# Kernel optimization log

Hardware: AMD Instinct MI355X
Metric: run time of the kernel (lower is better)

Reference implementation:

```python
import jax, jax.numpy as jnp
import numpy as np

HEADS = 32
DK = 32            # att_size = hidden // heads
CUT = 15.5         # tot_dis[cur_layer=0] + 0.5
NEG = -1e8
LN_EPS = 1e-5


def layernorm(x, g, b):
    m = jnp.mean(x, axis=-1, keepdims=True)
    v = jnp.mean((x - m) ** 2, axis=-1, keepdims=True)
    return (x - m) / jnp.sqrt(v + LN_EPS) * g + b


def setup_inputs() -> dict:
    key = jax.random.key(0)
    ks = jax.random.split(key, 12)
    B, S, H, F = 8, 513, 1024, 4096
    N = S - 1
    def nrm(k, shape, scale=0.02):
        return jax.random.normal(k, shape, jnp.float32) * scale
    x = jax.random.normal(ks[0], (B, S, H), jnp.float32)
    attn_bias = jax.random.normal(ks[1], (B, HEADS, S, S), jnp.float32)
    rel_pos = jax.random.randint(ks[2], (B, N, N), 0, 16, jnp.int32)
    rel_emb = nrm(ks[3], (512, HEADS)).at[0].set(0.0)  # padding_idx=0
    Wq = nrm(ks[4], (H, H)); bq = jnp.zeros((H,), jnp.float32)
    Wk = nrm(ks[5], (H, H)); bk = jnp.zeros((H,), jnp.float32)
    Wv = nrm(ks[6], (H, H)); bv = jnp.zeros((H,), jnp.float32)
    Wo = nrm(ks[7], (H, H)); bo = jnp.zeros((H,), jnp.float32)
    W1 = nrm(ks[8], (H, F)); b1 = jnp.zeros((F,), jnp.float32)
    W2 = nrm(ks[9], (F, H)); b2 = jnp.zeros((H,), jnp.float32)
    ln1_g = jnp.ones((H,), jnp.float32); ln1_b = jnp.zeros((H,), jnp.float32)
    ln2_g = jnp.ones((H,), jnp.float32); ln2_b = jnp.zeros((H,), jnp.float32)
    return dict(x=x, attn_bias=attn_bias, rel_emb=rel_emb,
                Wq=Wq, bq=bq, Wk=Wk, bk=bk, Wv=Wv, bv=bv, Wo=Wo, bo=bo,
                W1=W1, b1=b1, W2=W2, b2=b2,
                ln1_g=ln1_g, ln1_b=ln1_b, ln2_g=ln2_g, ln2_b=ln2_b,
                rel_pos=rel_pos)


def reference(x, attn_bias, rel_emb, Wq, bq, Wk, bk, Wv, bv, Wo, bo,
              W1, b1, W2, b2, ln1_g, ln1_b, ln2_g, ln2_b, rel_pos):
    B, S, H = x.shape
    # rel-pos bias: embed [B,N,N] -> [B,N,N,heads] -> [B,heads,N,N]
    rpb = jnp.transpose(rel_emb[rel_pos], (0, 3, 1, 2))
    inner = attn_bias[:, :, 1:, 1:] + rpb
    # per-head mask flag: keep if within cutoff distance OR already -inf-masked
    flags = (rel_pos[:, None, :, :] <= CUT) | (inner < NEG)
    ab = attn_bias.at[:, :, 1:, 1:].set(inner * flags)
    # attention
    y = layernorm(x, ln1_g, ln1_b)
    scale = DK ** -0.5
    q = (y @ Wq + bq).reshape(B, S, HEADS, DK) * scale
    k = (y @ Wk + bk).reshape(B, S, HEADS, DK)
    v = (y @ Wv + bv).reshape(B, S, HEADS, DK)
    scores = jnp.einsum('bqhd,bkhd->bhqk', q, k) + ab
    attn = jax.nn.softmax(scores, axis=-1)
    o = jnp.einsum('bhqk,bkhd->bqhd', attn, v).reshape(B, S, H)
    x = x + (o @ Wo + bo)
    # FFN
    y = layernorm(x, ln2_g, ln2_b)
    y = jax.nn.gelu(y @ W1 + b1, approximate=False) @ W2 + b2
    return x + y
```

## Files before the change

kernel.cpp:

```cpp
#include <hip/hip_runtime.h>
#include <hip/hip_bf16.h>
#include <math.h>

typedef __attribute__((ext_vector_type(8))) short short8;
typedef __attribute__((ext_vector_type(4))) float f32x4;
typedef unsigned short u16;
typedef unsigned int u32;

#define SQ 513
#define MPAD 4224
#define MV 4104
#define NHEADS 32
#define DKH 32
#define SVP 576

static __device__ inline u16 f2bf(float f) {
  u32 u = __builtin_bit_cast(u32, f);
  u = (u + 0x7fffu + ((u >> 16) & 1u)) >> 16;
  return (u16)u;
}

static __device__ inline void gld16(const void* g, void* l) {
  __builtin_amdgcn_global_load_lds((__attribute__((address_space(1))) void*)g,
                                   (__attribute__((address_space(3))) void*)l,
                                   16, 0, 0);
}

static __device__ inline float gelu_f(float x) {
  return 0.5f * x * (1.f + erff(x * 0.70710678118654752f));
}

__global__ __launch_bounds__(256) void transpose_cast_k(const float* __restrict__ in,
    u16* __restrict__ out, int K, int N, float scale)
{
  __shared__ float t[32][33];
  int n0 = blockIdx.x * 32, k0 = blockIdx.y * 32;
  int tx = threadIdx.x & 31, ty = threadIdx.x >> 5;
#pragma unroll
  for (int i = 0; i < 32; i += 8)
    t[ty + i][tx] = in[(size_t)(k0 + ty + i) * N + n0 + tx];
  __syncthreads();
#pragma unroll
  for (int i = 0; i < 32; i += 8)
    out[(size_t)(n0 + ty + i) * K + k0 + tx] = f2bf(t[tx][ty + i] * scale);
}

__global__ __launch_bounds__(256) void vtrans_k(const u16* __restrict__ qkv,
    u16* __restrict__ vT)
{
  __shared__ u16 t[32][33];
  int st = blockIdx.x * 32, h = blockIdx.y, b = blockIdx.z;
  int tx = threadIdx.x & 31, ty = threadIdx.x >> 5;
#pragma unroll
  for (int i = 0; i < 32; i += 8) {
    int s = st + ty + i;
    int sc = s > 512 ? 512 : s;
    t[ty + i][tx] = qkv[(size_t)(b * SQ + sc) * 3072 + 2048 + h * DKH + tx];
  }
  __syncthreads();
#pragma unroll
  for (int i = 0; i < 32; i += 8) {
    int d = ty + i;
    vT[(((size_t)b * NHEADS + h) * DKH + d) * SVP + st + tx] = t[tx][d];
  }
}

__global__ __launch_bounds__(256) void prep_bias_k(const float* __restrict__ bq,
    const float* __restrict__ bk, const float* __restrict__ bv,
    float* __restrict__ out, float scale)
{
  int i = blockIdx.x * 256 + threadIdx.x;
  float v = (i < 1024) ? bq[i] * scale : ((i < 2048) ? bk[i - 1024] : bv[i - 2048]);
  out[i] = v;
}

__global__ __launch_bounds__(256) void ln_k(const float* __restrict__ in,
    const float* __restrict__ g, const float* __restrict__ b,
    u16* __restrict__ out)
{
  int row = blockIdx.x;
  float4 v = ((const float4*)(in + (size_t)row * 1024))[threadIdx.x];
  float s = v.x + v.y + v.z + v.w;
  float s2 = v.x * v.x + v.y * v.y + v.z * v.z + v.w * v.w;
#pragma unroll
  for (int d = 32; d; d >>= 1) { s += __shfl_xor(s, d, 64); s2 += __shfl_xor(s2, d, 64); }
  __shared__ float ps[4], ps2[4];
  int w = threadIdx.x >> 6;
  if ((threadIdx.x & 63) == 0) { ps[w] = s; ps2[w] = s2; }
  __syncthreads();
  s = ps[0] + ps[1] + ps[2] + ps[3];
  s2 = ps2[0] + ps2[1] + ps2[2] + ps2[3];
  float mean = s * (1.f / 1024.f);
  float var = s2 * (1.f / 1024.f) - mean * mean;
  float inv = rsqrtf(var + 1e-5f);
  float4 gv = ((const float4*)g)[threadIdx.x];
  float4 bv = ((const float4*)b)[threadIdx.x];
  ushort4 o;
  o.x = f2bf((v.x - mean) * inv * gv.x + bv.x);
  o.y = f2bf((v.y - mean) * inv * gv.y + bv.y);
  o.z = f2bf((v.z - mean) * inv * gv.z + bv.z);
  o.w = f2bf((v.w - mean) * inv * gv.w + bv.w);
  ((ushort4*)(out + (size_t)row * 1024))[threadIdx.x] = o;
}

template <int EPI>
__global__ __launch_bounds__(256) void gemm_bt(const u16* __restrict__ A,
    const u16* __restrict__ Bw, const float* __restrict__ bias,
    const float* __restrict__ resid, void* __restrict__ outp,
    int N, int K, int nbx)
{
  __shared__ alignas(16) u16 sA[128 * 64];
  __shared__ alignas(16) u16 sB[128 * 64];
  int tid = threadIdx.x;
  int l = tid & 63, lg = l >> 4, li = l & 15;

  int bidx = blockIdx.x;
  int kbeg = 0, kend = K;
  float* pout = (float*)outp;
  if (EPI == 4) {
    int half = gridDim.x >> 1;
    int s = bidx >= half;
    bidx -= s * half;
    kbeg = s * (K >> 1);
    kend = kbeg + (K >> 1);
    pout += (size_t)s * MPAD * 1024;
  }
  int mb = bidx / nbx, nb = bidx % nbx;
  int m0 = mb * 128, n0 = nb * 128;
  int wv = tid >> 6;
  int wr = wv >> 1, wc = wv & 1;
  f32x4 acc[4][4] = {};
  int r_ = tid >> 3, c_ = (tid & 7) * 8;
  const u16* Ag = A + (size_t)(m0 + r_) * K + c_;
  const u16* Bg = Bw + (size_t)(n0 + r_) * K + c_;
  u16* sAb = sA + (tid & 192) * 8;
  u16* sBb = sB + (tid & 192) * 8;

  for (int k0 = kbeg; k0 < kend; k0 += 64) {
    __syncthreads();
#pragma unroll
    for (int i = 0; i < 4; ++i) {
      gld16(Ag + (size_t)(i * 32) * K + k0, sAb + i * 2048);
      gld16(Bg + (size_t)(i * 32) * K + k0, sBb + i * 2048);
    }
    __syncthreads();
#pragma unroll
    for (int ks = 0; ks < 2; ++ks) {
      short8 af[4], bfr[4];
#pragma unroll
      for (int i = 0; i < 4; ++i)
        af[i] = *(const short8*)&sA[(64 * wr + 16 * i + li) * 64 + ks * 32 + lg * 8];
#pragma unroll
      for (int j = 0; j < 4; ++j)
        bfr[j] = *(const short8*)&sB[(64 * wc + 16 * j + li) * 64 + ks * 32 + lg * 8];
#pragma unroll
      for (int i = 0; i < 4; ++i)
#pragma unroll
        for (int j = 0; j < 4; ++j)
          acc[i][j] = __builtin_amdgcn_mfma_f32_16x16x32_bf16(af[i], bfr[j], acc[i][j], 0, 0, 0);
    }
  }

#pragma unroll
  for (int i = 0; i < 4; ++i) {
    int rb = m0 + 64 * wr + 16 * i + 4 * lg;
#pragma unroll
    for (int j = 0; j < 4; ++j) {
      int col = n0 + 64 * wc + 16 * j + li;
      float bia = (EPI == 4) ? 0.f : bias[col];
#pragma unroll
      for (int r = 0; r < 4; ++r) {
        int row = rb + r;
        float v = acc[i][j][r] + bia;
        if (EPI == 0) {
          ((u16*)outp)[(size_t)row * N + col] = f2bf(v);
        } else if (EPI == 2) {
          ((u16*)outp)[(size_t)row * N + col] = f2bf(gelu_f(v));
        } else {
          pout[(size_t)row * N + col] = v;
        }
      }
    }
  }
}

__global__ __launch_bounds__(256) void oproj_combine(const float* __restrict__ part,
    float* __restrict__ out, const float* __restrict__ bo, const float* __restrict__ x)
{
  size_t idx = (size_t)blockIdx.x * 256 + threadIdx.x;
  const float4* p0 = (const float4*)part;
  const float4* p1 = (const float4*)(part + (size_t)MPAD * 1024);
  float4 a = p0[idx], b = p1[idx];
  float4 bb = ((const float4*)bo)[idx & 255];
  float4 xx = ((const float4*)x)[idx];
  a.x += b.x + bb.x + xx.x;
  a.y += b.y + bb.y + xx.y;
  a.z += b.z + bb.z + xx.z;
  a.w += b.w + bb.w + xx.w;
  ((float4*)out)[idx] = a;
}

__global__ __launch_bounds__(256) void ffn2_combine(const float* __restrict__ part,
    float* __restrict__ out, const float* __restrict__ b2)
{
  size_t idx = (size_t)blockIdx.x * 256 + threadIdx.x;
  const float4* p0 = (const float4*)part;
  const float4* p1 = (const float4*)(part + (size_t)MPAD * 1024);
  float4 a = ((float4*)out)[idx];
  float4 x0 = p0[idx], x1 = p1[idx];
  float4 bb = ((const float4*)b2)[idx & 255];
  a.x += x0.x + x1.x + bb.x;
  a.y += x0.y + x1.y + bb.y;
  a.z += x0.z + x1.z + bb.z;
  a.w += x0.w + x1.w + bb.w;
  ((float4*)out)[idx] = a;
}

__global__ __launch_bounds__(256) void attn_fused(const u16* __restrict__ qkv,
    const u16* __restrict__ vT, const float* __restrict__ attn_bias,
    const int* __restrict__ rel_pos, const float* __restrict__ rel_emb,
    u16* __restrict__ o)
{
  __shared__ alignas(16) u16 k_lds[2][64 * 32];
  __shared__ alignas(16) u16 v_lds[2][32 * 64];
  __shared__ alignas(16) u16 p_lds[4][16][72];
  int bid = blockIdx.x;
  int qt = bid % 9, h = (bid / 9) % NHEADS, b = bid / (9 * NHEADS);
  int tid = threadIdx.x, wv = tid >> 6, l = tid & 63, lg = l >> 4, li = l & 15;
  int q0 = qt * 64;
  int sqb = q0 + 16 * wv + 4 * lg;

  short8 qfrag = *(const short8*)(qkv + (size_t)(b * SQ + q0 + 16 * wv + li) * 3072 + h * DKH + lg * 8);

  float tv = rel_emb[(size_t)li * NHEADS + h];

  const float* bias_row[4];
  const int* rp_row[4];
#pragma unroll
  for (int r = 0; r < 4; ++r) {
    int sq = sqb + r;
    int sqc = sq > 512 ? 512 : sq;
    bias_row[r] = attn_bias + (((size_t)b * NHEADS + h) * SQ + sqc) * SQ;
    int sqm = sq - 1; sqm = sqm < 0 ? 0 : (sqm > 511 ? 511 : sqm);
    rp_row[r] = rel_pos + ((size_t)b * 512 + sqm) * 512;
  }

  int krow = tid >> 2;
  int kchunk = (tid & 3) ^ ((tid >> 3) & 3);
  const u16* ksrc = qkv + (size_t)(b * SQ) * 3072 + 1024 + h * DKH + kchunk * 8;
  int vrow = tid >> 3;
  int vchunk = (tid & 7) ^ (vrow & 7);
  const u16* vsrc = vT + (((size_t)b * NHEADS + h) * DKH + vrow) * SVP + vchunk * 8;

  int koff[4], voff[4];
#pragma unroll
  for (int f = 0; f < 4; ++f)
    koff[f] = (16 * f + li) * 32 + ((lg ^ ((li >> 1) & 3)) * 8);
#pragma unroll
  for (int u = 0; u < 4; ++u) {
    int df = u >> 1, kk = u & 1;
    voff[u] = (16 * df + li) * 64 + (((kk * 4 + lg) ^ (li & 7)) * 8);
  }

  float pb[4][4];
  int pr[4][4];

  gld16(ksrc + (size_t)krow * 3072, (u16*)k_lds[0] + tid * 8);
  gld16(vsrc, (u16*)v_lds[0] + tid * 8);
  __builtin_amdgcn_sched_barrier(0);
#pragma unroll
  for (int f = 0; f < 4; ++f) {
    int sk = 16 * f + li;
    int skm = sk - 1; skm = skm < 0 ? 0 : skm;
#pragma unroll
    for (int r = 0; r < 4; ++r) {
      pb[f][r] = bias_row[r][sk];
      pr[f][r] = rp_row[r][skm];
    }
  }

  f32x4 o_acc[2] = {};
  float l_run[4] = {0.f, 0.f, 0.f, 0.f};

#pragma unroll 1
  for (int kt = 0; kt < 9; ++kt) {
    int cur = kt & 1;
    asm volatile("s_waitcnt vmcnt(32)" ::: "memory");
    __builtin_amdgcn_s_barrier();
    if (kt < 8) {
      int s = (kt + 1) * 64 + krow; if (s > 512) s = 512;
      gld16(ksrc + (size_t)s * 3072, (u16*)k_lds[cur ^ 1] + tid * 8);
      gld16(vsrc + (size_t)(kt + 1) * 64, (u16*)v_lds[cur ^ 1] + tid * 8);
    }
    __builtin_amdgcn_sched_barrier(0);
    const u16* kb = k_lds[cur];
    const u16* vbf = v_lds[cur];

    f32x4 sc[4];
    __builtin_amdgcn_s_setprio(1);
#pragma unroll
    for (int f = 0; f < 4; ++f) {
      short8 kf = *(const short8*)&kb[koff[f]];
      f32x4 z = {};
      sc[f] = __builtin_amdgcn_mfma_f32_16x16x32_bf16(qfrag, kf, z, 0, 0, 0);
    }
    __builtin_amdgcn_s_setprio(0);

#pragma unroll
    for (int f = 0; f < 4; ++f) {
      int sk = kt * 64 + 16 * f + li;
#pragma unroll
      for (int r = 0; r < 4; ++r) {
        int sq = sqb + r;
        float base = pb[f][r];
        int rp = pr[f][r];
        float re = __shfl(tv, rp, 64);
        float inner = base + re;
        float ab = (rp <= 15 || inner < -1e8f) ? inner : 0.f;
        if (sq == 0 || sk == 0) ab = base;
        if (sq > 512 || sk > 512) ab = -1e30f;
        sc[f][r] += ab;
      }
    }
    if (kt < 8) {
#pragma unroll
      for (int f = 0; f < 4; ++f) {
        int sk = (kt + 1) * 64 + 16 * f + li;
        int skc = sk > 512 ? 512 : sk;
        int skm = sk - 1; skm = skm > 511 ? 511 : skm;
#pragma unroll
        for (int r = 0; r < 4; ++r) {
          pb[f][r] = bias_row[r][skc];
          pr[f][r] = rp_row[r][skm];
        }
      }
    }

#pragma unroll
    for (int f = 0; f < 4; ++f)
#pragma unroll
      for (int r = 0; r < 4; ++r) {
        float p = __expf(sc[f][r]);
        l_run[r] += p;
        p_lds[wv][4 * lg + r][16 * f + li] = f2bf(p);
      }

    __builtin_amdgcn_s_setprio(1);
#pragma unroll
    for (int kk = 0; kk < 2; ++kk) {
      short8 pa = *(const short8*)&p_lds[wv][li][kk * 32 + lg * 8];
#pragma unroll
      for (int df = 0; df < 2; ++df) {
        short8 vb = *(const short8*)&vbf[voff[df * 2 + kk]];
        o_acc[df] = __builtin_amdgcn_mfma_f32_16x16x32_bf16(pa, vb, o_acc[df], 0, 0, 0);
      }
    }
    __builtin_amdgcn_s_setprio(0);
  }

#pragma unroll
  for (int r = 0; r < 4; ++r) {
    float s = l_run[r];
#pragma unroll
    for (int d = 1; d < 16; d <<= 1) s += __shfl_xor(s, d, 16);
    l_run[r] = s;
  }
#pragma unroll
  for (int df = 0; df < 2; ++df)
#pragma unroll
    for (int r = 0; r < 4; ++r) {
      int s_q = sqb + r;
      if (s_q <= 512)
        o[(size_t)(b * SQ + s_q) * 1024 + h * DKH + 16 * df + li] = f2bf(o_acc[df][r] / l_run[r]);
    }
}

extern "C" void kernel_launch(void* const* d_in, const int* in_sizes, int n_in,
                              void* d_out, int out_size, void* d_ws, size_t ws_size,
                              hipStream_t stream) {
  const float* x        = (const float*)d_in[0];
  const float* attn_bias= (const float*)d_in[1];
  const float* rel_emb  = (const float*)d_in[2];
  const float* Wq = (const float*)d_in[3];
  const float* bq = (const float*)d_in[4];
  const float* Wk = (const float*)d_in[5];
  const float* bk = (const float*)d_in[6];
  const float* Wv = (const float*)d_in[7];
  const float* bv = (const float*)d_in[8];
  const float* Wo = (const float*)d_in[9];
  const float* bo = (const float*)d_in[10];
  const float* W1 = (const float*)d_in[11];
  const float* b1 = (const float*)d_in[12];
  const float* W2 = (const float*)d_in[13];
  const float* b2 = (const float*)d_in[14];
  const float* ln1g = (const float*)d_in[15];
  const float* ln1b = (const float*)d_in[16];
  const float* ln2g = (const float*)d_in[17];
  const float* ln2b = (const float*)d_in[18];
  const int*   rel_pos = (const int*)d_in[19];
  float* out = (float*)d_out;

  char* ws = (char*)d_ws;
  size_t off = 0;
  auto alloc = [&](size_t bytes) { char* p = ws + off; off += (bytes + 255) & ~(size_t)255; return p; };
  u16* w_qkvT = (u16*)alloc((size_t)3072 * 1024 * 2);
  u16* w_oT   = (u16*)alloc((size_t)1024 * 1024 * 2);
  u16* w_1T   = (u16*)alloc((size_t)4096 * 1024 * 2);
  u16* w_2T   = (u16*)alloc((size_t)1024 * 4096 * 2);
  float* bias_qkv = (float*)alloc(3072 * 4);
  u16* ybuf = (u16*)alloc((size_t)MPAD * 1024 * 2);
  u16* obuf = (u16*)alloc((size_t)MPAD * 1024 * 2);
  u16* vTb  = (u16*)alloc((size_t)8 * NHEADS * DKH * SVP * 2);
  u16* big  = (u16*)alloc((size_t)MPAD * 4096 * 2);
  float* part = (float*)alloc((size_t)2 * MPAD * 1024 * 4);

  const float scale = 0.17677669529663689f;
  dim3 blk(256);

  transpose_cast_k<<<dim3(32, 32), blk, 0, stream>>>(Wq, w_qkvT, 1024, 1024, scale);
  transpose_cast_k<<<dim3(32, 32), blk, 0, stream>>>(Wk, w_qkvT + (size_t)1024 * 1024, 1024, 1024, 1.f);
  transpose_cast_k<<<dim3(32, 32), blk, 0, stream>>>(Wv, w_qkvT + (size_t)2048 * 1024, 1024, 1024, 1.f);
  transpose_cast_k<<<dim3(32, 32), blk, 0, stream>>>(Wo, w_oT, 1024, 1024, 1.f);
  transpose_cast_k<<<dim3(128, 32), blk, 0, stream>>>(W1, w_1T, 1024, 4096, 1.f);
  transpose_cast_k<<<dim3(32, 128), blk, 0, stream>>>(W2, w_2T, 4096, 1024, 1.f);
  prep_bias_k<<<12, blk, 0, stream>>>(bq, bk, bv, bias_qkv, scale);

  ln_k<<<MV, blk, 0, stream>>>(x, ln1g, ln1b, ybuf);
  gemm_bt<0><<<33 * 24, blk, 0, stream>>>(ybuf, w_qkvT, bias_qkv, nullptr, big, 3072, 1024, 24);
  vtrans_k<<<dim3(18, NHEADS, 8), blk, 0, stream>>>(big, vTb);
  attn_fused<<<8 * NHEADS * 9, blk, 0, stream>>>(big, vTb, attn_bias, rel_pos, rel_emb, obuf);
  gemm_bt<4><<<33 * 8 * 2, blk, 0, stream>>>(obuf, w_oT, bo, nullptr, part, 1024, 1024, 8);
  oproj_combine<<<MV, blk, 0, stream>>>(part, out, bo, x);
  ln_k<<<MV, blk, 0, stream>>>(out, ln2g, ln2b, ybuf);
  gemm_bt<2><<<33 * 32, blk, 0, stream>>>(ybuf, w_1T, b1, nullptr, big, 4096, 1024, 32);
  gemm_bt<4><<<33 * 8 * 2, blk, 0, stream>>>(big, w_2T, b2, nullptr, part, 1024, 4096, 8);
  ffn2_combine<<<MV, blk, 0, stream>>>(part, out, b2);
}
```

Measured before the change: 492.0 us.

## Split attention key range across two blocks and combine partial results

Each attention block now handles only half of the key tiles (0-4 or 5-8), which doubles the grid to improve occupancy and parallelism. It writes unnormalized fp32 partial outputs and row sums to workspace, and a new combine kernel adds them, normalizes and casts to bf16. The softmax uses plain exp without a running max, so partials can be added directly. This adds an extra kernel launch and fp32 partial traffic, and the pipeline wait is now a full __syncthreads with no explicit vmcnt.

```diff
diff --git a/kernel.cpp b/kernel.cpp
--- a/kernel.cpp
+++ b/kernel.cpp
@@ -13,6 +13,7 @@
 #define NHEADS 32
 #define DKH 32
 #define SVP 576
+#define SQP 576
 
 static __device__ inline u16 f2bf(float f) {
   u32 u = __builtin_bit_cast(u32, f);
@@ -216,16 +217,39 @@
   ((float4*)out)[idx] = a;
 }
 
+__global__ __launch_bounds__(256) void attn_combine(const float* __restrict__ opart,
+    const float* __restrict__ lpart, u16* __restrict__ o)
+{
+  int row = blockIdx.x;
+  int b = row / SQ, sq = row % SQ;
+  int t = threadIdx.x;
+  int h = t >> 3;
+  float l0 = lpart[((size_t)b * NHEADS + h) * SQP + sq];
+  float l1 = lpart[(((size_t)8 + b) * NHEADS + h) * SQP + sq];
+  float inv = 1.f / (l0 + l1);
+  float4 o0 = ((const float4*)(opart + ((size_t)b * SQP + sq) * 1024))[t];
+  float4 o1 = ((const float4*)(opart + (((size_t)8 + b) * SQP + sq) * 1024))[t];
+  ushort4 r;
+  r.x = f2bf((o0.x + o1.x) * inv);
+  r.y = f2bf((o0.y + o1.y) * inv);
+  r.z = f2bf((o0.z + o1.z) * inv);
+  r.w = f2bf((o0.w + o1.w) * inv);
+  ((ushort4*)(o + (size_t)row * 1024))[t] = r;
+}
+
 __global__ __launch_bounds__(256) void attn_fused(const u16* __restrict__ qkv,
     const u16* __restrict__ vT, const float* __restrict__ attn_bias,
     const int* __restrict__ rel_pos, const float* __restrict__ rel_emb,
-    u16* __restrict__ o)
+    float* __restrict__ opart, float* __restrict__ lpart)
 {
   __shared__ alignas(16) u16 k_lds[2][64 * 32];
   __shared__ alignas(16) u16 v_lds[2][32 * 64];
   __shared__ alignas(16) u16 p_lds[4][16][72];
   int bid = blockIdx.x;
-  int qt = bid % 9, h = (bid / 9) % NHEADS, b = bid / (9 * NHEADS);
+  int sh = bid & 1;
+  int t3 = bid >> 1;
+  int qt = t3 % 9, h = (t3 / 9) % NHEADS, b = t3 / (9 * NHEADS);
+  int kb = sh ? 5 : 0, ke = sh ? 9 : 5;
   int tid = threadIdx.x, wv = tid >> 6, l = tid & 63, lg = l >> 4, li = l & 15;
   int q0 = qt * 64;
   int sqb = q0 + 16 * wv + 4 * lg;
@@ -265,12 +289,11 @@
   float pb[4][4];
   int pr[4][4];
 
-  gld16(ksrc + (size_t)krow * 3072, (u16*)k_lds[0] + tid * 8);
-  gld16(vsrc, (u16*)v_lds[0] + tid * 8);
-  __builtin_amdgcn_sched_barrier(0);
+  gld16(ksrc + (size_t)(kb * 64 + krow) * 3072, (u16*)k_lds[0] + tid * 8);
+  gld16(vsrc + (size_t)(kb * 64), (u16*)v_lds[0] + tid * 8);
 #pragma unroll
   for (int f = 0; f < 4; ++f) {
-    int sk = 16 * f + li;
+    int sk = kb * 64 + 16 * f + li;
     int skm = sk - 1; skm = skm < 0 ? 0 : skm;
 #pragma unroll
     for (int r = 0; r < 4; ++r) {
@@ -283,24 +306,22 @@
   float l_run[4] = {0.f, 0.f, 0.f, 0.f};
 
 #pragma unroll 1
-  for (int kt = 0; kt < 9; ++kt) {
-    int cur = kt & 1;
-    asm volatile("s_waitcnt vmcnt(32)" ::: "memory");
-    __builtin_amdgcn_s_barrier();
-    if (kt < 8) {
+  for (int kt = kb; kt < ke; ++kt) {
+    int cur = (kt - kb) & 1;
+    __syncthreads();
+    if (kt + 1 < ke) {
       int s = (kt + 1) * 64 + krow; if (s > 512) s = 512;
       gld16(ksrc + (size_t)s * 3072, (u16*)k_lds[cur ^ 1] + tid * 8);
       gld16(vsrc + (size_t)(kt + 1) * 64, (u16*)v_lds[cur ^ 1] + tid * 8);
     }
-    __builtin_amdgcn_sched_barrier(0);
-    const u16* kb = k_lds[cur];
+    const u16* kbp = k_lds[cur];
     const u16* vbf = v_lds[cur];
 
     f32x4 sc[4];
     __builtin_amdgcn_s_setprio(1);
 #pragma unroll
     for (int f = 0; f < 4; ++f) {
-      short8 kf = *(const short8*)&kb[koff[f]];
+      short8 kf = *(const short8*)&kbp[koff[f]];
       f32x4 z = {};
       sc[f] = __builtin_amdgcn_mfma_f32_16x16x32_bf16(qfrag, kf, z, 0, 0, 0);
     }
@@ -322,7 +343,7 @@
         sc[f][r] += ab;
       }
     }
-    if (kt < 8) {
+    if (kt + 1 < ke) {
 #pragma unroll
       for (int f = 0; f < 4; ++f) {
         int sk = (kt + 1) * 64 + 16 * f + li;
@@ -365,14 +386,18 @@
     for (int d = 1; d < 16; d <<= 1) s += __shfl_xor(s, d, 16);
     l_run[r] = s;
   }
-#pragma unroll
-  for (int df = 0; df < 2; ++df)
-#pragma unroll
-    for (int r = 0; r < 4; ++r) {
-      int s_q = sqb + r;
-      if (s_q <= 512)
-        o[(size_t)(b * SQ + s_q) * 1024 + h * DKH + 16 * df + li] = f2bf(o_acc[df][r] / l_run[r]);
-    }
+  float* ob = opart + ((size_t)(sh * 8 + b) * SQP) * 1024 + h * DKH;
+#pragma unroll
+  for (int r = 0; r < 4; ++r) {
+    int s_q = sqb + r;
+    if (s_q <= 512) {
+#pragma unroll
+      for (int df = 0; df < 2; ++df)
+        ob[(size_t)s_q * 1024 + 16 * df + li] = o_acc[df][r];
+      if (li == 0)
+        lpart[(((size_t)sh * 8 + b) * NHEADS + h) * SQP + s_q] = l_run[r];
+    }
+  }
 }
 
 extern "C" void kernel_launch(void* const* d_in, const int* in_sizes, int n_in,
@@ -412,7 +437,9 @@
   u16* obuf = (u16*)alloc((size_t)MPAD * 1024 * 2);
   u16* vTb  = (u16*)alloc((size_t)8 * NHEADS * DKH * SVP * 2);
   u16* big  = (u16*)alloc((size_t)MPAD * 4096 * 2);
-  float* part = (float*)alloc((size_t)2 * MPAD * 1024 * 4);
+  float* part  = (float*)alloc((size_t)2 * MPAD * 1024 * 4);
+  float* opart = (float*)alloc((size_t)16 * SQP * 1024 * 4);
+  float* lpart = (float*)alloc((size_t)16 * NHEADS * SQP * 4);
 
   const float scale = 0.17677669529663689f;
   dim3 blk(256);
@@ -428,7 +455,8 @@
   ln_k<<<MV, blk, 0, stream>>>(x, ln1g, ln1b, ybuf);
   gemm_bt<0><<<33 * 24, blk, 0, stream>>>(ybuf, w_qkvT, bias_qkv, nullptr, big, 3072, 1024, 24);
   vtrans_k<<<dim3(18, NHEADS, 8), blk, 0, stream>>>(big, vTb);
-  attn_fused<<<8 * NHEADS * 9, blk, 0, stream>>>(big, vTb, attn_bias, rel_pos, rel_emb, obuf);
+  attn_fused<<<8 * NHEADS * 9 * 2, blk, 0, stream>>>(big, vTb, attn_bias, rel_pos, rel_emb, opart, lpart);
+  attn_combine<<<8 * SQ, blk, 0, stream>>>(opart, lpart, obuf);
   gemm_bt<4><<<33 * 8 * 2, blk, 0, stream>>>(obuf, w_oT, bo, nullptr, part, 1024, 1024, 8);
   oproj_combine<<<MV, blk, 0, stream>>>(part, out, bo, x);
   ln_k<<<MV, blk, 0, stream>>>(out, ln2g, ln2b, ybuf);
```

Measured after the change: 507.7 us. +3.2%, slower.

## Precompute masked attention bias as tiled fp16 and stream it into LDS

Applied to the files above, without the earlier changes.

Adds a prep kernel that folds the attention bias, relative-position embedding lookup and cutoff mask into one fp16 tensor laid out per 64-key tile. The attention kernel then streams these tiles into double-buffered LDS with global_load_lds instead of doing scattered fp32 bias and rel_pos loads and shuffles per element. It also swaps the MFMA operand order so each lane holds four consecutive keys, which allows vectorized bias reads and P stores. This costs an extra pass over the full bias tensor and clamps the bias to the fp16 range, which can change results where masked values sit near the limit.

```diff
diff --git a/kernel.cpp b/kernel.cpp
--- a/kernel.cpp
+++ b/kernel.cpp
@@ -13,6 +13,7 @@
 #define NHEADS 32
 #define DKH 32
 #define SVP 576
+#define SQP 576
 
 static __device__ inline u16 f2bf(float f) {
   u32 u = __builtin_bit_cast(u32, f);
@@ -20,6 +21,14 @@
   return (u16)u;
 }
 
+static __device__ inline u16 f2h(float f) {
+  _Float16 h = (_Float16)f;
+  return __builtin_bit_cast(u16, h);
+}
+static __device__ inline float h2f(u16 b) {
+  return (float)__builtin_bit_cast(_Float16, b);
+}
+
 static __device__ inline void gld16(const void* g, void* l) {
   __builtin_amdgcn_global_load_lds((__attribute__((address_space(1))) void*)g,
                                    (__attribute__((address_space(3))) void*)l,
@@ -62,6 +71,39 @@
   for (int i = 0; i < 32; i += 8) {
     int d = ty + i;
     vT[(((size_t)b * NHEADS + h) * DKH + d) * SVP + st + tx] = t[tx][d];
+  }
+}
+
+__global__ __launch_bounds__(256) void prep_ab(const float* __restrict__ attn_bias,
+    const int* __restrict__ rel_pos, const float* __restrict__ rel_emb,
+    u16* __restrict__ abt)
+{
+  int bh = blockIdx.x;
+  int b = bh >> 5, h = bh & 31;
+  int t = threadIdx.x;
+  const float* brow_base = attn_bias + ((size_t)bh * SQ) * SQ;
+#pragma unroll 1
+  for (int rl = 0; rl < 16; ++rl) {
+    int sq = blockIdx.y * 16 + rl;
+#pragma unroll
+    for (int cc = 0; cc < 3; ++cc) {
+      int sk = t + cc * 256;
+      if (sk >= SQP) continue;
+      float ab;
+      if (sq > 512 || sk > 512) ab = -30000.f;
+      else {
+        float base = brow_base[(size_t)sq * SQ + sk];
+        if (sq == 0 || sk == 0) ab = base;
+        else {
+          int rp = rel_pos[((size_t)b * 512 + sq - 1) * 512 + sk - 1];
+          float inner = base + rel_emb[(size_t)rp * NHEADS + h];
+          ab = (rp <= 15 || inner < -1e8f) ? inner : 0.f;
+          if (ab < -30000.f) ab = -30000.f;
+        }
+      }
+      int kt = sk >> 6, kp = sk & 63;
+      abt[(((size_t)bh * 9 + kt) * SQP + sq) * 64 + kp] = f2h(ab);
+    }
   }
 }
 
@@ -217,13 +259,14 @@
 }
 
 __global__ __launch_bounds__(256) void attn_fused(const u16* __restrict__ qkv,
-    const u16* __restrict__ vT, const float* __restrict__ attn_bias,
-    const int* __restrict__ rel_pos, const float* __restrict__ rel_emb,
+    const u16* __restrict__ vT, const u16* __restrict__ abt,
     u16* __restrict__ o)
 {
   __shared__ alignas(16) u16 k_lds[2][64 * 32];
   __shared__ alignas(16) u16 v_lds[2][32 * 64];
+  __shared__ alignas(16) u16 ab_lds[2][64 * 64];
   __shared__ alignas(16) u16 p_lds[4][16][72];
+  __shared__ float l_lds[4][16];
   int bid = blockIdx.x;
   int qt = bid % 9, h = (bid / 9) % NHEADS, b = bid / (9 * NHEADS);
   int tid = threadIdx.x, wv = tid >> 6, l = tid & 63, lg = l >> 4, li = l & 15;
@@ -231,19 +274,6 @@
   int sqb = q0 + 16 * wv + 4 * lg;
 
   short8 qfrag = *(const short8*)(qkv + (size_t)(b * SQ + q0 + 16 * wv + li) * 3072 + h * DKH + lg * 8);
-
-  float tv = rel_emb[(size_t)li * NHEADS + h];
-
-  const float* bias_row[4];
-  const int* rp_row[4];
-#pragma unroll
-  for (int r = 0; r < 4; ++r) {
-    int sq = sqb + r;
-    int sqc = sq > 512 ? 512 : sq;
-    bias_row[r] = attn_bias + (((size_t)b * NHEADS + h) * SQ + sqc) * SQ;
-    int sqm = sq - 1; sqm = sqm < 0 ? 0 : (sqm > 511 ? 511 : sqm);
-    rp_row[r] = rel_pos + ((size_t)b * 512 + sqm) * 512;
-  }
 
   int krow = tid >> 2;
   int kchunk = (tid & 3) ^ ((tid >> 3) & 3);
@@ -251,99 +281,77 @@
   int vrow = tid >> 3;
   int vchunk = (tid & 7) ^ (vrow & 7);
   const u16* vsrc = vT + (((size_t)b * NHEADS + h) * DKH + vrow) * SVP + vchunk * 8;
-
-  int koff[4], voff[4];
+  int abrow = tid >> 3;
+  int abcir = (tid & 7) ^ (abrow & 7);
+  const u16* absrc0 = abt + ((size_t)(b * NHEADS + h) * 9) * SQP * 64 + (size_t)q0 * 64
+                      + abrow * 64 + abcir * 8;
+
+  int koff[4];
 #pragma unroll
   for (int f = 0; f < 4; ++f)
     koff[f] = (16 * f + li) * 32 + ((lg ^ ((li >> 1) & 3)) * 8);
+  int voff[4];
 #pragma unroll
   for (int u = 0; u < 4; ++u) {
     int df = u >> 1, kk = u & 1;
     voff[u] = (16 * df + li) * 64 + (((kk * 4 + lg) ^ (li & 7)) * 8);
   }
-
-  float pb[4][4];
-  int pr[4][4];
+  int aboff[4];
+#pragma unroll
+  for (int f = 0; f < 4; ++f)
+    aboff[f] = (16 * wv + li) * 128 + (((2 * f + (lg >> 1)) ^ (li & 7)) << 4) + 8 * (lg & 1);
 
   gld16(ksrc + (size_t)krow * 3072, (u16*)k_lds[0] + tid * 8);
   gld16(vsrc, (u16*)v_lds[0] + tid * 8);
-  __builtin_amdgcn_sched_barrier(0);
-#pragma unroll
-  for (int f = 0; f < 4; ++f) {
-    int sk = 16 * f + li;
-    int skm = sk - 1; skm = skm < 0 ? 0 : skm;
-#pragma unroll
-    for (int r = 0; r < 4; ++r) {
-      pb[f][r] = bias_row[r][sk];
-      pr[f][r] = rp_row[r][skm];
-    }
-  }
+  gld16(absrc0, (u16*)ab_lds[0] + tid * 8);
+  gld16(absrc0 + 2048, (u16*)ab_lds[0] + 2048 + tid * 8);
 
   f32x4 o_acc[2] = {};
-  float l_run[4] = {0.f, 0.f, 0.f, 0.f};
+  float l_run = 0.f;
 
 #pragma unroll 1
   for (int kt = 0; kt < 9; ++kt) {
     int cur = kt & 1;
-    asm volatile("s_waitcnt vmcnt(32)" ::: "memory");
-    __builtin_amdgcn_s_barrier();
+    __syncthreads();
     if (kt < 8) {
       int s = (kt + 1) * 64 + krow; if (s > 512) s = 512;
       gld16(ksrc + (size_t)s * 3072, (u16*)k_lds[cur ^ 1] + tid * 8);
       gld16(vsrc + (size_t)(kt + 1) * 64, (u16*)v_lds[cur ^ 1] + tid * 8);
-    }
-    __builtin_amdgcn_sched_barrier(0);
-    const u16* kb = k_lds[cur];
+      const u16* abn = absrc0 + (size_t)(kt + 1) * SQP * 64;
+      gld16(abn, (u16*)ab_lds[cur ^ 1] + tid * 8);
+      gld16(abn + 2048, (u16*)ab_lds[cur ^ 1] + 2048 + tid * 8);
+    }
+    const u16* kbp = k_lds[cur];
     const u16* vbf = v_lds[cur];
+    const char* abl = (const char*)ab_lds[cur];
 
     f32x4 sc[4];
     __builtin_amdgcn_s_setprio(1);
 #pragma unroll
     for (int f = 0; f < 4; ++f) {
-      short8 kf = *(const short8*)&kb[koff[f]];
+      short8 kf = *(const short8*)&kbp[koff[f]];
       f32x4 z = {};
-      sc[f] = __builtin_amdgcn_mfma_f32_16x16x32_bf16(qfrag, kf, z, 0, 0, 0);
+      sc[f] = __builtin_amdgcn_mfma_f32_16x16x32_bf16(kf, qfrag, z, 0, 0, 0);
     }
     __builtin_amdgcn_s_setprio(0);
 
 #pragma unroll
     for (int f = 0; f < 4; ++f) {
-      int sk = kt * 64 + 16 * f + li;
-#pragma unroll
-      for (int r = 0; r < 4; ++r) {
-        int sq = sqb + r;
-        float base = pb[f][r];
-        int rp = pr[f][r];
-        float re = __shfl(tv, rp, 64);
-        float inner = base + re;
-        float ab = (rp <= 15 || inner < -1e8f) ? inner : 0.f;
-        if (sq == 0 || sk == 0) ab = base;
-        if (sq > 512 || sk > 512) ab = -1e30f;
-        sc[f][r] += ab;
-      }
-    }
-    if (kt < 8) {
-#pragma unroll
-      for (int f = 0; f < 4; ++f) {
-        int sk = (kt + 1) * 64 + 16 * f + li;
-        int skc = sk > 512 ? 512 : sk;
-        int skm = sk - 1; skm = skm > 511 ? 511 : skm;
-#pragma unroll
-        for (int r = 0; r < 4; ++r) {
-          pb[f][r] = bias_row[r][skc];
-          pr[f][r] = rp_row[r][skm];
-        }
-      }
-    }
-
-#pragma unroll
-    for (int f = 0; f < 4; ++f)
-#pragma unroll
-      for (int r = 0; r < 4; ++r) {
-        float p = __expf(sc[f][r]);
-        l_run[r] += p;
-        p_lds[wv][4 * lg + r][16 * f + li] = f2bf(p);
-      }
+      uint2 uu = *(const uint2*)(abl + aboff[f]);
+      float a0 = h2f((u16)(uu.x & 0xffffu));
+      float a1 = h2f((u16)(uu.x >> 16));
+      float a2 = h2f((u16)(uu.y & 0xffffu));
+      float a3 = h2f((u16)(uu.y >> 16));
+      float p0 = __expf(sc[f][0] + a0);
+      float p1 = __expf(sc[f][1] + a1);
+      float p2 = __expf(sc[f][2] + a2);
+      float p3 = __expf(sc[f][3] + a3);
+      l_run += (p0 + p1) + (p2 + p3);
+      uint2 pk;
+      pk.x = (u32)f2bf(p0) | ((u32)f2bf(p1) << 16);
+      pk.y = (u32)f2bf(p2) | ((u32)f2bf(p3) << 16);
+      *(uint2*)((char*)&p_lds[wv][0][0] + li * 144 + f * 32 + lg * 8) = pk;
+    }
 
     __builtin_amdgcn_s_setprio(1);
 #pragma unroll
@@ -358,20 +366,20 @@
     __builtin_amdgcn_s_setprio(0);
   }
 
-#pragma unroll
-  for (int r = 0; r < 4; ++r) {
-    float s = l_run[r];
-#pragma unroll
-    for (int d = 1; d < 16; d <<= 1) s += __shfl_xor(s, d, 16);
-    l_run[r] = s;
-  }
+  float s = l_run;
+  s += __shfl_xor(s, 16, 64);
+  s += __shfl_xor(s, 32, 64);
+  if (l < 16) l_lds[wv][l] = s;
+  float lr[4];
+#pragma unroll
+  for (int r = 0; r < 4; ++r) lr[r] = l_lds[wv][4 * lg + r];
 #pragma unroll
   for (int df = 0; df < 2; ++df)
 #pragma unroll
     for (int r = 0; r < 4; ++r) {
       int s_q = sqb + r;
       if (s_q <= 512)
-        o[(size_t)(b * SQ + s_q) * 1024 + h * DKH + 16 * df + li] = f2bf(o_acc[df][r] / l_run[r]);
+        o[(size_t)(b * SQ + s_q) * 1024 + h * DKH + 16 * df + li] = f2bf(o_acc[df][r] / lr[r]);
     }
 }
 
@@ -413,10 +421,12 @@
   u16* vTb  = (u16*)alloc((size_t)8 * NHEADS * DKH * SVP * 2);
   u16* big  = (u16*)alloc((size_t)MPAD * 4096 * 2);
   float* part = (float*)alloc((size_t)2 * MPAD * 1024 * 4);
+  u16* abt  = (u16*)alloc((size_t)256 * 9 * SQP * 64 * 2);
 
   const float scale = 0.17677669529663689f;
   dim3 blk(256);
 
+  prep_ab<<<dim3(256, 36), blk, 0, stream>>>(attn_bias, rel_pos, rel_emb, abt);
   transpose_cast_k<<<dim3(32, 32), blk, 0, stream>>>(Wq, w_qkvT, 1024, 1024, scale);
   transpose_cast_k<<<dim3(32, 32), blk, 0, stream>>>(Wk, w_qkvT + (size_t)1024 * 1024, 1024, 1024, 1.f);
   transpose_cast_k<<<dim3(32, 32), blk, 0, stream>>>(Wv, w_qkvT + (size_t)2048 * 1024, 1024, 1024, 1.f);
@@ -428,7 +438,7 @@
   ln_k<<<MV, blk, 0, stream>>>(x, ln1g, ln1b, ybuf);
   gemm_bt<0><<<33 * 24, blk, 0, stream>>>(ybuf, w_qkvT, bias_qkv, nullptr, big, 3072, 1024, 24);
   vtrans_k<<<dim3(18, NHEADS, 8), blk, 0, stream>>>(big, vTb);
-  attn_fused<<<8 * NHEADS * 9, blk, 0, stream>>>(big, vTb, attn_bias, rel_pos, rel_emb, obuf);
+  attn_fused<<<8 * NHEADS * 9, blk, 0, stream>>>(big, vTb, abt, obuf);
   gemm_bt<4><<<33 * 8 * 2, blk, 0, stream>>>(obuf, w_oT, bo, nullptr, part, 1024, 1024, 8);
   oproj_combine<<<MV, blk, 0, stream>>>(part, out, bo, x);
   ln_k<<<MV, blk, 0, stream>>>(out, ln2g, ln2b, ybuf);
```

New measurement: 605.2 us. +23.0%, slower.
